# Performance work log

Hardware: AMD Instinct MI355X
Metric: run time of the kernel (lower is better)

The kernel has to match this reference:

```python
import jax, jax.numpy as jnp
import numpy as np

B, S, D, H = 4, 1024, 1024, 16
DK = D // H


def setup_inputs() -> dict:
    rng = jax.random.key(0)
    ks = jax.random.split(rng, 12)
    w_scale = 1.0 / np.sqrt(D)
    return {
        "query": jax.random.normal(ks[0], (B, S, D), jnp.float32),
        "key": jax.random.normal(ks[1], (B, S, D), jnp.float32),
        "mask": jax.random.randint(ks[2], (B, S, S), 0, 2, jnp.int32),
        "aspect": jax.random.normal(ks[3], (B, D), jnp.float32),
        "short": jax.random.normal(ks[4], (B, H, S, S), jnp.float32),
        # linears[0] (query proj) and linears[1] (key proj): Linear(d_model, d_model)
        "Wq": jax.random.uniform(ks[5], (D, D), jnp.float32, -w_scale, w_scale),
        "bq": jax.random.uniform(ks[6], (D,), jnp.float32, -w_scale, w_scale),
        "Wk": jax.random.uniform(ks[7], (D, D), jnp.float32, -w_scale, w_scale),
        "bk": jax.random.uniform(ks[8], (D,), jnp.float32, -w_scale, w_scale),
        # dense: Linear(d_model, d_k)
        "Wd": jax.random.uniform(ks[9], (DK, D), jnp.float32, -w_scale, w_scale),
        "bd": jax.random.uniform(ks[10], (DK,), jnp.float32, -w_scale, w_scale),
        # weight_m ~ randn(h, d_k, d_k), bias_m = ones(1) as in the torch module
        "weight_m": jax.random.normal(ks[11], (H, DK, DK), jnp.float32),
        "bias_m": jnp.ones((1,), jnp.float32),
    }


def reference(query, key, mask, aspect, short, Wq, bq, Wk, bk, Wd, bd, weight_m, bias_m):
    b, sq, d = query.shape
    h, dk, _ = weight_m.shape
    # projections -> [b, h, s, dk]
    q = (jnp.einsum('bsd,ed->bse', query, Wq) + bq).reshape(b, sq, h, dk).transpose(0, 2, 1, 3)
    k = (jnp.einsum('bsd,ed->bse', key, Wk) + bk).reshape(b, -1, h, dk).transpose(0, 2, 1, 3)
    # scaled QK^T: [b, h, sq, sk]
    scores = jnp.einsum('bhqd,bhkd->bhqk', q, k) / jnp.sqrt(jnp.asarray(dk, q.dtype))
    # aspect path: the torch code expands aspect over heads BEFORE the shared
    # dense layer, so the per-head aspect vector is identical -> [b, dk]
    asp = jnp.einsum('bd,ed->be', aspect, Wd) + bd
    # aspect . weight_m : [b, h, dk]; then dot with keys -> [b, h, sk]
    aw = jnp.einsum('bc,hcd->bhd', asp, weight_m)
    aspect_scores = jnp.tanh(jnp.einsum('bhd,bhkd->bhk', aw, k) + bias_m[0])
    # constant along query axis -> broadcast instead of materializing [b,h,sq,sk]
    scores = scores + aspect_scores[:, :, None, :] + short
    m = mask[:, :, :sq][:, None, :, :]  # [b, 1, sq, sk]
    scores = jnp.where(m == 0, jnp.asarray(-1e9, scores.dtype), scores)
    return jax.nn.softmax(scores, axis=-1)
```

## Files before the change

kernel.cpp:

```cpp
#include <hip/hip_runtime.h>

typedef unsigned short u16;
typedef __bf16 bf16x8 __attribute__((ext_vector_type(8)));
typedef float f32x4 __attribute__((ext_vector_type(4)));
typedef u16 u16x8 __attribute__((ext_vector_type(8)));

#define NB 4
#define NS 1024
#define ND 1024
#define NH 16
#define NDK 64

__device__ __forceinline__ u16 f2bf(float f) {
    unsigned int u = __float_as_uint(f);
    return (u16)((u + 0x7FFFu + ((u >> 16) & 1u)) >> 16);
}

__global__ __launch_bounds__(256) void conv_kernel(const float* __restrict__ src,
                                                   u16* __restrict__ dst) {
    int idx = blockIdx.x * 256 + threadIdx.x;
    const float4* s4 = (const float4*)src + (size_t)idx * 2;
    float4 a = s4[0], c = s4[1];
    u16x8 o;
    o[0] = f2bf(a.x); o[1] = f2bf(a.y); o[2] = f2bf(a.z); o[3] = f2bf(a.w);
    o[4] = f2bf(c.x); o[5] = f2bf(c.y); o[6] = f2bf(c.z); o[7] = f2bf(c.w);
    *((u16x8*)dst + idx) = o;
}

__global__ __launch_bounds__(256) void proj_kernel(
    const u16* __restrict__ qbf, const u16* __restrict__ kbf,
    const u16* __restrict__ wqbf, const u16* __restrict__ wkbf,
    const float* __restrict__ bq, const float* __restrict__ bk,
    u16* __restrict__ qp, u16* __restrict__ kp) {
    const u16* X = blockIdx.z ? kbf : qbf;
    const u16* W = blockIdx.z ? wkbf : wqbf;
    const float* bias = blockIdx.z ? bk : bq;
    u16* O = blockIdx.z ? kp : qp;

    const int n0 = blockIdx.x * 64;
    const int m0 = blockIdx.y * 128;

    __shared__ u16 Xs[128][72];
    __shared__ u16 Ws[64][72];

    const int t = threadIdx.x;
    const int l = t & 63, w = t >> 6;
    const int lr = l & 15, lh = l >> 4;
    const int wm = w * 32;

    f32x4 zero = {0.f, 0.f, 0.f, 0.f};
    f32x4 acc[2][4];
    for (int mi = 0; mi < 2; mi++)
        for (int nj = 0; nj < 4; nj++) acc[mi][nj] = zero;

    const int sr = t >> 3;
    const int sc8 = (t & 7) * 8;

    for (int k0 = 0; k0 < ND; k0 += 64) {
        for (int p = 0; p < 4; p++) {
            uint4 v = *(const uint4*)(X + (size_t)(m0 + sr + p * 32) * ND + k0 + sc8);
            *(uint4*)&Xs[sr + p * 32][sc8] = v;
        }
        for (int p = 0; p < 2; p++) {
            uint4 v = *(const uint4*)(W + (size_t)(n0 + sr + p * 32) * ND + k0 + sc8);
            *(uint4*)&Ws[sr + p * 32][sc8] = v;
        }
        __syncthreads();
        for (int kk = 0; kk < 2; kk++) {
            const int ko = kk * 32 + lh * 8;
            bf16x8 a[2], bb[4];
            for (int mi = 0; mi < 2; mi++)
                a[mi] = *(const bf16x8*)&Xs[wm + mi * 16 + lr][ko];
            for (int nj = 0; nj < 4; nj++)
                bb[nj] = *(const bf16x8*)&Ws[nj * 16 + lr][ko];
            for (int mi = 0; mi < 2; mi++)
                for (int nj = 0; nj < 4; nj++)
                    acc[mi][nj] = __builtin_amdgcn_mfma_f32_16x16x32_bf16(
                        a[mi], bb[nj], acc[mi][nj], 0, 0, 0);
        }
        __syncthreads();
    }
    for (int mi = 0; mi < 2; mi++)
        for (int nj = 0; nj < 4; nj++)
            for (int r = 0; r < 4; r++) {
                int row = m0 + wm + mi * 16 + lh * 4 + r;
                int col = n0 + nj * 16 + lr;
                float v = acc[mi][nj][r] + bias[col];
                O[(size_t)row * ND + col] = f2bf(v);
            }
}

__global__ __launch_bounds__(256) void aspect_kernel(
    const float* __restrict__ aspect, const float* __restrict__ Wd,
    const float* __restrict__ bd, const float* __restrict__ wm,
    const float* __restrict__ bm, const float* __restrict__ Wk,
    const float* __restrict__ bk, const float* __restrict__ key,
    float* __restrict__ asps) {
    __shared__ float red[256];
    __shared__ float sAsp[64];
    __shared__ float sAw[64];
    __shared__ float sV[1024];

    const int bid = blockIdx.x;
    const int sq = bid & 3, h = (bid >> 2) & 15, b = bid >> 6;
    const int t = threadIdx.x;

    {
        int c = t & 63, part = t >> 6;
        const float* ar = aspect + b * ND + part * 256;
        const float* wr = Wd + (size_t)c * ND + part * 256;
        float acc = 0.f;
        for (int i = 0; i < 256; i++) acc += ar[i] * wr[i];
        red[t] = acc;
    }
    __syncthreads();
    if (t < 64) sAsp[t] = red[t] + red[t + 64] + red[t + 128] + red[t + 192] + bd[t];
    __syncthreads();
    {
        int dp = t & 63, part = t >> 6;
        float acc = 0.f;
        for (int c = part * 16; c < part * 16 + 16; c++)
            acc += sAsp[c] * wm[((size_t)h * 64 + c) * 64 + dp];
        red[t] = acc;
    }
    __syncthreads();
    if (t < 64) sAw[t] = red[t] + red[t + 64] + red[t + 128] + red[t + 192];
    __syncthreads();
    {
        float a0 = 0.f, a1 = 0.f, a2 = 0.f, a3 = 0.f;
        for (int c = 0; c < 64; c++) {
            float aw = sAw[c];
            const float* wkr = Wk + ((size_t)h * 64 + c) * ND;
            a0 += aw * wkr[t];
            a1 += aw * wkr[t + 256];
            a2 += aw * wkr[t + 512];
            a3 += aw * wkr[t + 768];
        }
        sV[t] = a0; sV[t + 256] = a1; sV[t + 512] = a2; sV[t + 768] = a3;
    }
    float c0 = bm[0];
    for (int c = 0; c < 64; c++) c0 += sAw[c] * bk[h * 64 + c];
    __syncthreads();
    const int s = sq * 256 + t;
    const float4* kr = (const float4*)(key + ((size_t)b * NS + s) * ND);
    const float4* vr = (const float4*)sV;
    float acc = 0.f;
    for (int i = 0; i < 256; i++) {
        float4 kv = kr[i], vv = vr[i];
        acc += kv.x * vv.x + kv.y * vv.y + kv.z * vv.z + kv.w * vv.w;
    }
    asps[((size_t)b * NH + h) * NS + s] = tanhf(acc + c0);
}

__global__ __launch_bounds__(256) void attn_kernel(
    const u16* __restrict__ qp, const u16* __restrict__ kp,
    const float* __restrict__ asps, const float* __restrict__ shrt,
    const int* __restrict__ maskp, float* __restrict__ out) {
    __shared__ float sc[16][1024];

    const int bid = blockIdx.x;
    const int b = bid >> 10;
    const int rb = (bid >> 4) & 63;
    const int h = bid & 15;
    const int t = threadIdx.x;
    const int l = t & 63, w = t >> 6;
    const int lr = l & 15, lh = l >> 4;

    const u16* qbase = qp + ((size_t)(b * NS + rb * 16 + lr)) * ND + h * 64 + lh * 8;
    bf16x8 a0 = *(const bf16x8*)(qbase);
    bf16x8 a1 = *(const bf16x8*)(qbase + 32);

    f32x4 zero = {0.f, 0.f, 0.f, 0.f};
    for (int i = 0; i < 16; i++) {
        int ct = w * 16 + i;
        const u16* kbase = kp + ((size_t)(b * NS + ct * 16 + lr)) * ND + h * 64 + lh * 8;
        bf16x8 b0 = *(const bf16x8*)(kbase);
        bf16x8 b1 = *(const bf16x8*)(kbase + 32);
        f32x4 acc = zero;
        acc = __builtin_amdgcn_mfma_f32_16x16x32_bf16(a0, b0, acc, 0, 0, 0);
        acc = __builtin_amdgcn_mfma_f32_16x16x32_bf16(a1, b1, acc, 0, 0, 0);
        int col = ct * 16 + lr;
        for (int r = 0; r < 4; r++) sc[lh * 4 + r][col] = acc[r] * 0.125f;
    }
    __syncthreads();

    const size_t bh = (size_t)(b * NH + h);
    const float* arow = asps + bh * NS;
    for (int r4 = 0; r4 < 4; r4++) {
        int row = w * 4 + r4;
        int qrow = rb * 16 + row;
        const float* srow = shrt + (bh * NS + qrow) * NS;
        const int* mrow = maskp + ((size_t)b * NS + qrow) * NS;
        float v[16];
        float m = -3e38f;
        for (int i = 0; i < 16; i++) {
            int c = l + i * 64;
            float s = sc[row][c] + srow[c] + arow[c];
            s = (mrow[c] == 0) ? -1e9f : s;
            v[i] = s;
            m = fmaxf(m, s);
        }
        for (int o = 1; o < 64; o <<= 1) m = fmaxf(m, __shfl_xor(m, o, 64));
        float sum = 0.f;
        for (int i = 0; i < 16; i++) {
            v[i] = __expf(v[i] - m);
            sum += v[i];
        }
        for (int o = 1; o < 64; o <<= 1) sum += __shfl_xor(sum, o, 64);
        float inv = 1.0f / sum;
        float* orow = out + (bh * NS + qrow) * NS;
        for (int i = 0; i < 16; i++) orow[l + i * 64] = v[i] * inv;
    }
}

extern "C" void kernel_launch(void* const* d_in, const int* in_sizes, int n_in,
                              void* d_out, int out_size, void* d_ws, size_t ws_size,
                              hipStream_t stream) {
    const float* query  = (const float*)d_in[0];
    const float* key    = (const float*)d_in[1];
    const int*   maskp  = (const int*)d_in[2];
    const float* aspect = (const float*)d_in[3];
    const float* shrt   = (const float*)d_in[4];
    const float* Wq     = (const float*)d_in[5];
    const float* bq     = (const float*)d_in[6];
    const float* Wk     = (const float*)d_in[7];
    const float* bk     = (const float*)d_in[8];
    const float* Wd     = (const float*)d_in[9];
    const float* bd     = (const float*)d_in[10];
    const float* wm     = (const float*)d_in[11];
    const float* bm     = (const float*)d_in[12];
    float* out = (float*)d_out;

    char* ws = (char*)d_ws;
    const size_t M4 = (size_t)4 * 1024 * 1024;
    const size_t M1 = (size_t)1024 * 1024;
    u16* qbf  = (u16*)ws;
    u16* kbf  = qbf + M4;
    u16* wqbf = kbf + M4;
    u16* wkbf = wqbf + M1;
    u16* qp   = wkbf + M1;
    u16* kp   = qp + M4;
    float* asps = (float*)(kp + M4);

    conv_kernel<<<2048, 256, 0, stream>>>(query, qbf);
    conv_kernel<<<2048, 256, 0, stream>>>(key, kbf);
    conv_kernel<<<512, 256, 0, stream>>>(Wq, wqbf);
    conv_kernel<<<512, 256, 0, stream>>>(Wk, wkbf);

    proj_kernel<<<dim3(16, 32, 2), 256, 0, stream>>>(qbf, kbf, wqbf, wkbf, bq, bk, qp, kp);

    aspect_kernel<<<256, 256, 0, stream>>>(aspect, Wd, bd, wm, bm, Wk, bk, key, asps);

    attn_kernel<<<4096, 256, 0, stream>>>(qp, kp, asps, shrt, maskp, out);
}
```

Measured before the change: 700.6 us.

## Split aspect scoring to share key reads across heads; retile projection GEMM

The aspect path is split into two kernels. A small kernel builds the per-(batch, head) vector from Wd, weight_m and Wk. A second kernel reads each key row once and scores it against all 16 heads from LDS, so the key tensor is no longer re-read once per head. The projection GEMM moves to 128x128 tiles filled through global_load_lds. The attention/softmax kernel now uses 512 threads with float4/int4 vectorized loads and stores. The trade-offs are one extra launch, larger LDS use per block (64 KB in aspect_score), and more registers per thread in the GEMM.

```diff
diff --git a/kernel.cpp b/kernel.cpp
--- a/kernel.cpp
+++ b/kernel.cpp
@@ -14,6 +14,13 @@
 __device__ __forceinline__ u16 f2bf(float f) {
     unsigned int u = __float_as_uint(f);
     return (u16)((u + 0x7FFFu + ((u >> 16) & 1u)) >> 16);
+}
+
+typedef __attribute__((address_space(3))) unsigned int as3_u32;
+typedef __attribute__((address_space(1))) const unsigned int as1_u32;
+
+__device__ __forceinline__ void gload_lds16(const u16* g, u16* lds) {
+    __builtin_amdgcn_global_load_lds((as1_u32*)g, (as3_u32*)lds, 16, 0, 0);
 }
 
 __global__ __launch_bounds__(256) void conv_kernel(const float* __restrict__ src,
@@ -37,94 +44,88 @@
     const float* bias = blockIdx.z ? bk : bq;
     u16* O = blockIdx.z ? kp : qp;
 
-    const int n0 = blockIdx.x * 64;
+    const int n0 = blockIdx.x * 128;
     const int m0 = blockIdx.y * 128;
 
-    __shared__ u16 Xs[128][72];
-    __shared__ u16 Ws[64][72];
+    __shared__ u16 As[128 * 64];
+    __shared__ u16 Bs[128 * 64];
 
     const int t = threadIdx.x;
     const int l = t & 63, w = t >> 6;
     const int lr = l & 15, lh = l >> 4;
-    const int wm = w * 32;
-
-    f32x4 zero = {0.f, 0.f, 0.f, 0.f};
-    f32x4 acc[2][4];
-    for (int mi = 0; mi < 2; mi++)
-        for (int nj = 0; nj < 4; nj++) acc[mi][nj] = zero;
-
-    const int sr = t >> 3;
-    const int sc8 = (t & 7) * 8;
+    const int wr = (w >> 1) * 64, wc = (w & 1) * 64;
+
+    const int srow = w * 8 + (l >> 3);
+    const int scol = (l & 7) * 8;
+
+    f32x4 acc[4][4];
+    for (int mi = 0; mi < 4; mi++)
+        for (int nj = 0; nj < 4; nj++) acc[mi][nj] = (f32x4){0.f, 0.f, 0.f, 0.f};
 
     for (int k0 = 0; k0 < ND; k0 += 64) {
         for (int p = 0; p < 4; p++) {
-            uint4 v = *(const uint4*)(X + (size_t)(m0 + sr + p * 32) * ND + k0 + sc8);
-            *(uint4*)&Xs[sr + p * 32][sc8] = v;
-        }
-        for (int p = 0; p < 2; p++) {
-            uint4 v = *(const uint4*)(W + (size_t)(n0 + sr + p * 32) * ND + k0 + sc8);
-            *(uint4*)&Ws[sr + p * 32][sc8] = v;
+            gload_lds16(X + (size_t)(m0 + srow + p * 32) * ND + k0 + scol,
+                        As + (w * 8 + p * 32) * 64);
+            gload_lds16(W + (size_t)(n0 + srow + p * 32) * ND + k0 + scol,
+                        Bs + (w * 8 + p * 32) * 64);
         }
         __syncthreads();
         for (int kk = 0; kk < 2; kk++) {
             const int ko = kk * 32 + lh * 8;
-            bf16x8 a[2], bb[4];
-            for (int mi = 0; mi < 2; mi++)
-                a[mi] = *(const bf16x8*)&Xs[wm + mi * 16 + lr][ko];
+            bf16x8 a[4], b[4];
+            for (int mi = 0; mi < 4; mi++)
+                a[mi] = *(const bf16x8*)&As[(wr + mi * 16 + lr) * 64 + ko];
             for (int nj = 0; nj < 4; nj++)
-                bb[nj] = *(const bf16x8*)&Ws[nj * 16 + lr][ko];
-            for (int mi = 0; mi < 2; mi++)
+                b[nj] = *(const bf16x8*)&Bs[(wc + nj * 16 + lr) * 64 + ko];
+            for (int mi = 0; mi < 4; mi++)
                 for (int nj = 0; nj < 4; nj++)
                     acc[mi][nj] = __builtin_amdgcn_mfma_f32_16x16x32_bf16(
-                        a[mi], bb[nj], acc[mi][nj], 0, 0, 0);
+                        a[mi], b[nj], acc[mi][nj], 0, 0, 0);
         }
         __syncthreads();
     }
-    for (int mi = 0; mi < 2; mi++)
-        for (int nj = 0; nj < 4; nj++)
+    for (int nj = 0; nj < 4; nj++) {
+        int col = n0 + wc + nj * 16 + lr;
+        float bv = bias[col];
+        for (int mi = 0; mi < 4; mi++)
             for (int r = 0; r < 4; r++) {
-                int row = m0 + wm + mi * 16 + lh * 4 + r;
-                int col = n0 + nj * 16 + lr;
-                float v = acc[mi][nj][r] + bias[col];
-                O[(size_t)row * ND + col] = f2bf(v);
+                int row = m0 + wr + mi * 16 + lh * 4 + r;
+                O[(size_t)row * ND + col] = f2bf(acc[mi][nj][r] + bv);
             }
-}
-
-__global__ __launch_bounds__(256) void aspect_kernel(
+    }
+}
+
+__global__ __launch_bounds__(256) void aspect_pre(
     const float* __restrict__ aspect, const float* __restrict__ Wd,
     const float* __restrict__ bd, const float* __restrict__ wm,
     const float* __restrict__ bm, const float* __restrict__ Wk,
-    const float* __restrict__ bk, const float* __restrict__ key,
-    float* __restrict__ asps) {
-    __shared__ float red[256];
+    const float* __restrict__ bk, float* __restrict__ vout,
+    float* __restrict__ c0out) {
     __shared__ float sAsp[64];
     __shared__ float sAw[64];
-    __shared__ float sV[1024];
-
     const int bid = blockIdx.x;
-    const int sq = bid & 3, h = (bid >> 2) & 15, b = bid >> 6;
-    const int t = threadIdx.x;
-
-    {
-        int c = t & 63, part = t >> 6;
-        const float* ar = aspect + b * ND + part * 256;
-        const float* wr = Wd + (size_t)c * ND + part * 256;
+    const int h = bid & 15, b = bid >> 4;
+    const int t = threadIdx.x, l = t & 63, w = t >> 6;
+
+    const float4* ar = (const float4*)(aspect + (size_t)b * ND);
+    for (int ci = 0; ci < 16; ci++) {
+        int c = w * 16 + ci;
+        const float4* wr4 = (const float4*)(Wd + (size_t)c * ND);
         float acc = 0.f;
-        for (int i = 0; i < 256; i++) acc += ar[i] * wr[i];
-        red[t] = acc;
+        for (int j = 0; j < 4; j++) {
+            float4 av = ar[l + j * 64], wv = wr4[l + j * 64];
+            acc += av.x * wv.x + av.y * wv.y + av.z * wv.z + av.w * wv.w;
+        }
+        for (int o = 1; o < 64; o <<= 1) acc += __shfl_xor(acc, o, 64);
+        if (l == 0) sAsp[c] = acc + bd[c];
     }
     __syncthreads();
-    if (t < 64) sAsp[t] = red[t] + red[t + 64] + red[t + 128] + red[t + 192] + bd[t];
-    __syncthreads();
-    {
-        int dp = t & 63, part = t >> 6;
+    if (t < 64) {
         float acc = 0.f;
-        for (int c = part * 16; c < part * 16 + 16; c++)
-            acc += sAsp[c] * wm[((size_t)h * 64 + c) * 64 + dp];
-        red[t] = acc;
-    }
-    __syncthreads();
-    if (t < 64) sAw[t] = red[t] + red[t + 64] + red[t + 128] + red[t + 192];
+        for (int c = 0; c < 64; c++)
+            acc += sAsp[c] * wm[((size_t)h * 64 + c) * 64 + t];
+        sAw[t] = acc;
+    }
     __syncthreads();
     {
         float a0 = 0.f, a1 = 0.f, a2 = 0.f, a3 = 0.f;
@@ -136,27 +137,64 @@
             a2 += aw * wkr[t + 512];
             a3 += aw * wkr[t + 768];
         }
-        sV[t] = a0; sV[t + 256] = a1; sV[t + 512] = a2; sV[t + 768] = a3;
-    }
-    float c0 = bm[0];
-    for (int c = 0; c < 64; c++) c0 += sAw[c] * bk[h * 64 + c];
+        float* vo = vout + ((size_t)b * NH + h) * ND;
+        vo[t] = a0; vo[t + 256] = a1; vo[t + 512] = a2; vo[t + 768] = a3;
+    }
+    if (t == 0) {
+        float c0 = bm[0];
+        for (int c = 0; c < 64; c++) c0 += sAw[c] * bk[h * 64 + c];
+        c0out[b * NH + h] = c0;
+    }
+}
+
+__global__ __launch_bounds__(256) void aspect_score(
+    const float* __restrict__ key, const float* __restrict__ vin,
+    const float* __restrict__ c0in, float* __restrict__ asps) {
+    __shared__ float vs[16 * 1024];
+    const int bid = blockIdx.x;
+    const int chunk = bid & 63, b = bid >> 6;
+    const int t = threadIdx.x, l = t & 63, w = t >> 6;
+
+    const float4* vg = (const float4*)(vin + (size_t)b * NH * ND);
+    float4* vl = (float4*)vs;
+    for (int j = 0; j < 16; j++) vl[t + j * 256] = vg[t + j * 256];
     __syncthreads();
-    const int s = sq * 256 + t;
-    const float4* kr = (const float4*)(key + ((size_t)b * NS + s) * ND);
-    const float4* vr = (const float4*)sV;
-    float acc = 0.f;
-    for (int i = 0; i < 256; i++) {
-        float4 kv = kr[i], vv = vr[i];
-        acc += kv.x * vv.x + kv.y * vv.y + kv.z * vv.z + kv.w * vv.w;
-    }
-    asps[((size_t)b * NH + h) * NS + s] = tanhf(acc + c0);
-}
-
-__global__ __launch_bounds__(256) void attn_kernel(
+
+    for (int r = 0; r < 4; r++) {
+        int s = chunk * 16 + w * 4 + r;
+        const float4* kr = (const float4*)(key + ((size_t)b * NS + s) * ND);
+        float4 kx[4];
+        for (int j = 0; j < 4; j++) kx[j] = kr[l + j * 64];
+        float ph[16];
+#pragma unroll
+        for (int h = 0; h < 16; h++) {
+            const float4* vh = (const float4*)(vs + h * 1024);
+            float acc = 0.f;
+            for (int j = 0; j < 4; j++) {
+                float4 vv = vh[l + j * 64];
+                acc += kx[j].x * vv.x + kx[j].y * vv.y + kx[j].z * vv.z + kx[j].w * vv.w;
+            }
+            ph[h] = acc;
+        }
+#pragma unroll
+        for (int o = 1; o < 64; o <<= 1)
+#pragma unroll
+            for (int h = 0; h < 16; h++) ph[h] += __shfl_xor(ph[h], o, 64);
+        if (l < 16) {
+            float val = ph[0];
+#pragma unroll
+            for (int h = 1; h < 16; h++)
+                if (l == h) val = ph[h];
+            asps[((size_t)b * NH + l) * NS + s] = tanhf(val + c0in[b * NH + l]);
+        }
+    }
+}
+
+__global__ __launch_bounds__(512, 4) void attn_kernel(
     const u16* __restrict__ qp, const u16* __restrict__ kp,
     const float* __restrict__ asps, const float* __restrict__ shrt,
     const int* __restrict__ maskp, float* __restrict__ out) {
-    __shared__ float sc[16][1024];
+    __shared__ float sc[16 * 1024];
 
     const int bid = blockIdx.x;
     const int b = bid >> 10;
@@ -170,46 +208,66 @@
     bf16x8 a0 = *(const bf16x8*)(qbase);
     bf16x8 a1 = *(const bf16x8*)(qbase + 32);
 
-    f32x4 zero = {0.f, 0.f, 0.f, 0.f};
-    for (int i = 0; i < 16; i++) {
-        int ct = w * 16 + i;
+    for (int i = 0; i < 8; i++) {
+        int ct = w * 8 + i;
         const u16* kbase = kp + ((size_t)(b * NS + ct * 16 + lr)) * ND + h * 64 + lh * 8;
         bf16x8 b0 = *(const bf16x8*)(kbase);
         bf16x8 b1 = *(const bf16x8*)(kbase + 32);
-        f32x4 acc = zero;
+        f32x4 acc = {0.f, 0.f, 0.f, 0.f};
         acc = __builtin_amdgcn_mfma_f32_16x16x32_bf16(a0, b0, acc, 0, 0, 0);
         acc = __builtin_amdgcn_mfma_f32_16x16x32_bf16(a1, b1, acc, 0, 0, 0);
         int col = ct * 16 + lr;
-        for (int r = 0; r < 4; r++) sc[lh * 4 + r][col] = acc[r] * 0.125f;
+        for (int r = 0; r < 4; r++) sc[(lh * 4 + r) * 1024 + col] = acc[r] * 0.125f;
     }
     __syncthreads();
 
-    const size_t bh = (size_t)(b * NH + h);
-    const float* arow = asps + bh * NS;
-    for (int r4 = 0; r4 < 4; r4++) {
-        int row = w * 4 + r4;
+    const size_t bh = (size_t)b * NH + h;
+    const float4* ar4 = (const float4*)(asps + bh * NS);
+    for (int rr = 0; rr < 2; rr++) {
+        int row = w * 2 + rr;
         int qrow = rb * 16 + row;
-        const float* srow = shrt + (bh * NS + qrow) * NS;
-        const int* mrow = maskp + ((size_t)b * NS + qrow) * NS;
-        float v[16];
+        const float4* srow = (const float4*)(shrt + (bh * NS + qrow) * NS);
+        const int4*  mrow = (const int4*)(maskp + ((size_t)b * NS + qrow) * NS);
+        const float4* scr = (const float4*)(sc + row * 1024);
+        float4 v[4];
         float m = -3e38f;
-        for (int i = 0; i < 16; i++) {
-            int c = l + i * 64;
-            float s = sc[row][c] + srow[c] + arow[c];
-            s = (mrow[c] == 0) ? -1e9f : s;
-            v[i] = s;
-            m = fmaxf(m, s);
-        }
+#pragma unroll
+        for (int j = 0; j < 4; j++) {
+            int f = l + j * 64;
+            float4 s4 = scr[f];
+            float4 sh4 = srow[f];
+            float4 a4 = ar4[f];
+            int4 m4 = mrow[f];
+            float4 x;
+            x.x = (m4.x == 0) ? -1e9f : s4.x + sh4.x + a4.x;
+            x.y = (m4.y == 0) ? -1e9f : s4.y + sh4.y + a4.y;
+            x.z = (m4.z == 0) ? -1e9f : s4.z + sh4.z + a4.z;
+            x.w = (m4.w == 0) ? -1e9f : s4.w + sh4.w + a4.w;
+            v[j] = x;
+            m = fmaxf(m, fmaxf(fmaxf(x.x, x.y), fmaxf(x.z, x.w)));
+        }
+#pragma unroll
         for (int o = 1; o < 64; o <<= 1) m = fmaxf(m, __shfl_xor(m, o, 64));
         float sum = 0.f;
-        for (int i = 0; i < 16; i++) {
-            v[i] = __expf(v[i] - m);
-            sum += v[i];
-        }
+#pragma unroll
+        for (int j = 0; j < 4; j++) {
+            v[j].x = __expf(v[j].x - m);
+            v[j].y = __expf(v[j].y - m);
+            v[j].z = __expf(v[j].z - m);
+            v[j].w = __expf(v[j].w - m);
+            sum += v[j].x + v[j].y + v[j].z + v[j].w;
+        }
+#pragma unroll
         for (int o = 1; o < 64; o <<= 1) sum += __shfl_xor(sum, o, 64);
         float inv = 1.0f / sum;
-        float* orow = out + (bh * NS + qrow) * NS;
-        for (int i = 0; i < 16; i++) orow[l + i * 64] = v[i] * inv;
+        float4* orow = (float4*)(out + (bh * NS + qrow) * NS);
+#pragma unroll
+        for (int j = 0; j < 4; j++) {
+            float4 o4;
+            o4.x = v[j].x * inv; o4.y = v[j].y * inv;
+            o4.z = v[j].z * inv; o4.w = v[j].w * inv;
+            orow[l + j * 64] = o4;
+        }
     }
 }
 
@@ -241,15 +299,18 @@
     u16* qp   = wkbf + M1;
     u16* kp   = qp + M4;
     float* asps = (float*)(kp + M4);
+    float* vbuf = asps + (size_t)NB * NH * NS;
+    float* c0buf = vbuf + (size_t)NB * NH * ND;
 
     conv_kernel<<<2048, 256, 0, stream>>>(query, qbf);
     conv_kernel<<<2048, 256, 0, stream>>>(key, kbf);
     conv_kernel<<<512, 256, 0, stream>>>(Wq, wqbf);
     conv_kernel<<<512, 256, 0, stream>>>(Wk, wkbf);
 
-    proj_kernel<<<dim3(16, 32, 2), 256, 0, stream>>>(qbf, kbf, wqbf, wkbf, bq, bk, qp, kp);
-
-    aspect_kernel<<<256, 256, 0, stream>>>(aspect, Wd, bd, wm, bm, Wk, bk, key, asps);
-
-    attn_kernel<<<4096, 256, 0, stream>>>(qp, kp, asps, shrt, maskp, out);
-}
+    proj_kernel<<<dim3(8, 32, 2), 256, 0, stream>>>(qbf, kbf, wqbf, wkbf, bq, bk, qp, kp);
+
+    aspect_pre<<<64, 256, 0, stream>>>(aspect, Wd, bd, wm, bm, Wk, bk, vbuf, c0buf);
+    aspect_score<<<256, 256, 0, stream>>>(key, vbuf, c0buf, asps);
+
+    attn_kernel<<<4096, 512, 0, stream>>>(qp, kp, asps, shrt, maskp, out);
+}
```

Measured after the change: 666.1 us. -4.9%, faster.
